# Kernel tuning notes

Measured on AMD Instinct MI355X. Metric: run time of the kernel, lower is better.

The kernel has to match this reference:

```python
import jax, jax.numpy as jnp
import numpy as np

B, M, N, L = 4096, 128, 96, 20


def setup_inputs() -> dict:
    key = jax.random.key(0)
    k1, k2, k3, k4 = jax.random.split(key, 4)
    x_ini = jax.random.normal(k1, (B, N, 1), jnp.float32)
    y = jax.random.normal(k2, (B, M, 1), jnp.float32)
    H = jax.random.normal(k3, (B, M, N), jnp.float32)
    xt = jax.random.normal(k4, (B, N, 1), jnp.float32)
    # learned parameters, initialized exactly as in the torch __init__
    grad_ss = jnp.full((L,), 0.001, jnp.float32)
    extra = []
    t = 1.0
    for _ in range(L):
        t1 = (1.0 + np.sqrt(1.0 + 4.0 * t * t)) / 2.0
        extra.append((t - 1.0) / t1)
        t = t1
    extra_ss = jnp.asarray(np.array(extra, dtype=np.float32))
    gamma1 = jnp.asarray(np.array([(5.0 - 0.1) / L * i + 0.1 for i in range(L)], dtype=np.float32))
    return {"x_ini": x_ini, "y": y, "H": H, "xt": xt,
            "grad_ss": grad_ss, "extra_ss": extra_ss, "gamma1": gamma1}


def reference(x_ini, y, H, xt, grad_ss, extra_ss, gamma1):
    central = jnp.array([-2.0, 0.0, 2.0], dtype=x_ini.dtype)  # 3-point codebook
    HTH = jnp.einsum('bmn,bmk->bnk', H, H)   # [B,N,N]
    HTy = jnp.einsum('bmn,bmk->bnk', H, y)   # [B,N,1]

    def step(carry, params):
        x, y_x = carry
        gs, es, gm = params
        grad_f = 2.0 * (jnp.matmul(HTH, y_x) - HTy)          # [B,N,1]
        x_buff = y_x - gs * grad_f                            # [B,N,1]
        # nearest-center lookup over the 3-entry codebook
        idx = jnp.argmin(jnp.abs(x_buff - central[None, None, :]), axis=2)  # [B,N]
        center = central[idx][..., None]                      # [B,N,1]
        ply = 2.0 * jax.nn.sigmoid(gm * (x_buff - center)) - 1.0
        y_x_new = ply + es * (ply - x)                        # FISTA momentum
        return (ply, y_x_new), None

    (x, _), _ = jax.lax.scan(step, (x_ini, x_ini), (grad_ss, extra_ss, gamma1))
    d = x - xt
    loss = jnp.sum(d * d).reshape(1, 1)  # sum_b (x-xt)^T (x-xt)
    return x, loss
```

## Files before the change

### kernel.cpp

```cpp
#include <hip/hip_runtime.h>

#define NB 4096
#define MM 128
#define NN 96
#define LL 20

typedef __attribute__((ext_vector_type(8))) short bf16x8;
typedef __attribute__((ext_vector_type(4))) float f32x4;
typedef __attribute__((ext_vector_type(4))) unsigned int u32x4;

#define UT_STRIDE 72

__device__ __forceinline__ unsigned short rne16(float f) {
    unsigned u = __float_as_uint(f);
    return (unsigned short)((u + 0x7fffu + ((u >> 16) & 1u)) >> 16);
}
__device__ __forceinline__ unsigned pack2(float a, float b) {
    return (unsigned)rne16(a) | ((unsigned)rne16(b) << 16);
}
__device__ __forceinline__ float bperm_f(int srcB, float v) {
    return __int_as_float(__builtin_amdgcn_ds_bpermute(srcB, __float_as_int(v)));
}

__global__ __launch_bounds__(64) __attribute__((amdgpu_waves_per_eu(2)))
void pg_kernel(const float* __restrict__ x_ini,
               const float* __restrict__ y,
               const float* __restrict__ H,
               const float* __restrict__ xt,
               const float* __restrict__ grad_ss,
               const float* __restrict__ extra_ss,
               const float* __restrict__ gamma1,
               float* __restrict__ out)
{
    __shared__ __align__(16) unsigned short Ut[112 * UT_STRIDE];
    __shared__ __align__(16) unsigned yxL[48];
    __shared__ float par[3][LL];

    const int b    = blockIdx.x;
    const int lane = threadIdx.x;
    const int m15  = lane & 15;
    const int g4   = lane >> 4;

    if (lane < LL) {
        par[0][lane] = grad_ss[lane];
        par[1][lane] = extra_ss[lane];
        par[2][lane] = gamma1[lane];
    }
    {
        unsigned* U32 = (unsigned*)Ut;
        #pragma unroll
        for (int i = 97 * (UT_STRIDE / 2) + lane; i < 112 * (UT_STRIDE / 2); i += 64)
            U32[i] = 0;
    }

    f32x4 acc[6][7];
    #pragma unroll
    for (int I = 0; I < 6; ++I)
        #pragma unroll
        for (int J = 0; J < 7; ++J)
            #pragma unroll
            for (int r = 0; r < 4; ++r) acc[I][J][r] = 0.f;

    const float* Hb = H + (size_t)b * (MM * NN);
    for (int kh = 0; kh < 2; ++kh) {
        if (kh) __syncthreads();
        const float* rsrc = Hb + (size_t)(kh * 64 + lane) * NN;
        #pragma unroll
        for (int ch = 0; ch < 4; ++ch) {
            float4 v[6];
            #pragma unroll
            for (int i = 0; i < 6; ++i) v[i] = *(const float4*)(rsrc + ch * 24 + 4 * i);
            #pragma unroll
            for (int i = 0; i < 6; ++i) {
                const int c = ch * 24 + 4 * i;
                Ut[(c + 0) * UT_STRIDE + lane] = rne16(v[i].x);
                Ut[(c + 1) * UT_STRIDE + lane] = rne16(v[i].y);
                Ut[(c + 2) * UT_STRIDE + lane] = rne16(v[i].z);
                Ut[(c + 3) * UT_STRIDE + lane] = rne16(v[i].w);
            }
        }
        Ut[96 * UT_STRIDE + lane] = rne16(y[(size_t)b * MM + kh * 64 + lane]);
        __syncthreads();

        #pragma unroll
        for (int s = 0; s < 2; ++s) {
            bf16x8 fr[7];
            #pragma unroll
            for (int T = 0; T < 7; ++T)
                fr[T] = *(const bf16x8*)&Ut[(T * 16 + m15) * UT_STRIDE + s * 32 + g4 * 8];
            #pragma unroll
            for (int I = 0; I < 6; ++I)
                #pragma unroll
                for (int J = 0; J < 7; ++J)
                    acc[I][J] = __builtin_amdgcn_mfma_f32_16x16x32_bf16(fr[I], fr[J], acc[I][J], 0, 0, 0);
        }
    }

    unsigned pk[6][6][2];
    #pragma unroll
    for (int I = 0; I < 6; ++I)
        #pragma unroll
        for (int J = 0; J < 6; ++J) {
            pk[I][J][0] = pack2(acc[I][J][0], acc[I][J][1]);
            pk[I][J][1] = pack2(acc[I][J][2], acc[I][J][3]);
        }
    const int srcL[2] = { (m15 + 16 * (2 * (g4 & 1) + 0)) << 2,
                          (m15 + 16 * (2 * (g4 & 1) + 1)) << 2 };
    const bool hiHalf = (g4 >> 1) != 0;
    bf16x8 afr[6][3];
    #pragma unroll
    for (int Ip = 0; Ip < 6; ++Ip)
        #pragma unroll
        for (int kk = 0; kk < 3; ++kk) {
            u32x4 w;
            #pragma unroll
            for (int p = 0; p < 4; ++p) {
                int va = __builtin_amdgcn_ds_bpermute(srcL[p >> 1], (int)pk[2 * kk][Ip][p & 1]);
                int vb = __builtin_amdgcn_ds_bpermute(srcL[p >> 1], (int)pk[2 * kk + 1][Ip][p & 1]);
                w[p] = (unsigned)(hiHalf ? vb : va);
            }
            afr[Ip][kk] = __builtin_bit_cast(bf16x8, w);
        }
    float hty4[4];
    {
        const int srcC = (16 * g4) << 2;
        #pragma unroll
        for (int r = 0; r < 4; ++r) {
            float v0 = bperm_f(srcC, acc[0][6][r]);
            float v1 = bperm_f(srcC, acc[1][6][r]);
            float v2 = bperm_f(srcC, acc[2][6][r]);
            float v3 = bperm_f(srcC, acc[3][6][r]);
            float v4 = bperm_f(srcC, acc[4][6][r]);
            float v5 = bperm_f(srcC, acc[5][6][r]);
            float s = v0;
            s = (m15 == 1) ? v1 : s;
            s = (m15 == 2) ? v2 : s;
            s = (m15 == 3) ? v3 : s;
            s = (m15 == 4) ? v4 : s;
            s = (m15 == 5) ? v5 : s;
            hty4[r] = s;
        }
    }

    const bool wr = (m15 < 6);
    const int  rb = m15 * 16 + g4 * 4;
    float yx4[4] = {0, 0, 0, 0}, xc4[4] = {0, 0, 0, 0};
    if (wr) {
        float4 xi = *(const float4*)(x_ini + (size_t)b * NN + rb);
        yx4[0] = xi.x; yx4[1] = xi.y; yx4[2] = xi.z; yx4[3] = xi.w;
        xc4[0] = xi.x; xc4[1] = xi.y; xc4[2] = xi.z; xc4[3] = xi.w;
        yxL[(rb >> 1) + 0] = pack2(yx4[0], yx4[1]);
        yxL[(rb >> 1) + 1] = pack2(yx4[2], yx4[3]);
    }
    __syncthreads();

    for (int t = 0; t < LL; ++t) {
        bf16x8 bf[3];
        #pragma unroll
        for (int kk = 0; kk < 3; ++kk)
            bf[kk] = *(const bf16x8*)&yxL[kk * 16 + g4 * 4];
        f32x4 aD[6];
        #pragma unroll
        for (int Ip = 0; Ip < 6; ++Ip)
            #pragma unroll
            for (int r = 0; r < 4; ++r) aD[Ip][r] = 0.f;
        #pragma unroll
        for (int kk = 0; kk < 3; ++kk)
            #pragma unroll
            for (int Ip = 0; Ip < 6; ++Ip)
                aD[Ip] = __builtin_amdgcn_mfma_f32_16x16x32_bf16(afr[Ip][kk], bf[kk], aD[Ip], 0, 0, 0);
        f32x4 am = aD[0];
        am = (m15 == 1) ? aD[1] : am;
        am = (m15 == 2) ? aD[2] : am;
        am = (m15 == 3) ? aD[3] : am;
        am = (m15 == 4) ? aD[4] : am;
        am = (m15 == 5) ? aD[5] : am;

        if (wr) {
            const float gs = par[0][t], es = par[1][t], gmv = par[2][t];
            #pragma unroll
            for (int r = 0; r < 4; ++r) {
                float xb  = fmaf(-2.0f * gs, am[r] - hty4[r], yx4[r]);
                float cen = 2.0f * fminf(fmaxf(rintf(xb * 0.5f), -1.0f), 1.0f);
                float z   = gmv * (xb - cen);
                float e   = __expf(-z);
                float ply = fmaf(2.0f, __builtin_amdgcn_rcpf(1.0f + e), -1.0f);
                float yxn = fmaf(es, ply - xc4[r], ply);
                xc4[r] = ply;
                yx4[r] = yxn;
            }
            if (t + 1 < LL) {
                yxL[(rb >> 1) + 0] = pack2(yx4[0], yx4[1]);
                yxL[(rb >> 1) + 1] = pack2(yx4[2], yx4[3]);
            }
        }
        __syncthreads();
    }

    float part = 0.f;
    if (wr) {
        float4 xo;
        xo.x = xc4[0]; xo.y = xc4[1]; xo.z = xc4[2]; xo.w = xc4[3];
        *(float4*)(out + (size_t)b * NN + rb) = xo;
        float4 xr = *(const float4*)(xt + (size_t)b * NN + rb);
        float d0 = xc4[0] - xr.x, d1 = xc4[1] - xr.y;
        float d2 = xc4[2] - xr.z, d3 = xc4[3] - xr.w;
        part = (d0 * d0 + d1 * d1) + (d2 * d2 + d3 * d3);
    }
    #pragma unroll
    for (int m = 1; m < 64; m <<= 1) part += __shfl_xor(part, m, 64);
    if (lane == 0) atomicAdd(out + (size_t)NB * NN, part);
}

extern "C" void kernel_launch(void* const* d_in, const int* in_sizes, int n_in,
                              void* d_out, int out_size, void* d_ws, size_t ws_size,
                              hipStream_t stream) {
    const float* x_ini    = (const float*)d_in[0];
    const float* y        = (const float*)d_in[1];
    const float* H        = (const float*)d_in[2];
    const float* xt       = (const float*)d_in[3];
    const float* grad_ss  = (const float*)d_in[4];
    const float* extra_ss = (const float*)d_in[5];
    const float* gamma1   = (const float*)d_in[6];
    float* out = (float*)d_out;

    hipMemsetAsync(out + (size_t)NB * NN, 0, sizeof(float), stream);
    pg_kernel<<<NB, 64, 0, stream>>>(x_ini, y, H, xt, grad_ss, extra_ss, gamma1, out);
}
```

Before: 96.23 us.

## Split per-batch Gram and iteration work across two waves per block

Each block now runs 128 threads (two waves). Each wave computes half of the HTH columns plus HTy through MFMA, then holds only its half of the matrix fragments for the 20 iterations. The y_x vector is double-buffered in shared memory so one barrier per iteration is enough across the waves. HTy now passes through shared memory instead of bpermute shuffles. This cuts per-wave MFMA and register load and should raise occupancy, at the cost of a cross-wave barrier in every iteration and duplicated A-fragment loads.

```diff
diff --git a/kernel.cpp b/kernel.cpp
--- a/kernel.cpp
+++ b/kernel.cpp
@@ -4,13 +4,12 @@
 #define MM 128
 #define NN 96
 #define LL 20
+#define UTS 72
 
 typedef __attribute__((ext_vector_type(8))) short bf16x8;
 typedef __attribute__((ext_vector_type(4))) float f32x4;
 typedef __attribute__((ext_vector_type(4))) unsigned int u32x4;
 
-#define UT_STRIDE 72
-
 __device__ __forceinline__ unsigned short rne16(float f) {
     unsigned u = __float_as_uint(f);
     return (unsigned short)((u + 0x7fffu + ((u >> 16) & 1u)) >> 16);
@@ -18,11 +17,8 @@
 __device__ __forceinline__ unsigned pack2(float a, float b) {
     return (unsigned)rne16(a) | ((unsigned)rne16(b) << 16);
 }
-__device__ __forceinline__ float bperm_f(int srcB, float v) {
-    return __int_as_float(__builtin_amdgcn_ds_bpermute(srcB, __float_as_int(v)));
-}
-
-__global__ __launch_bounds__(64) __attribute__((amdgpu_waves_per_eu(2)))
+
+__global__ __launch_bounds__(128) __attribute__((amdgpu_waves_per_eu(3)))
 void pg_kernel(const float* __restrict__ x_ini,
                const float* __restrict__ y,
                const float* __restrict__ H,
@@ -32,149 +28,150 @@
                const float* __restrict__ gamma1,
                float* __restrict__ out)
 {
-    __shared__ __align__(16) unsigned short Ut[112 * UT_STRIDE];
-    __shared__ __align__(16) unsigned yxL[48];
+    __shared__ __align__(16) unsigned short Ut[97 * UTS];
+    __shared__ __align__(16) unsigned yxD[2][48];
+    __shared__ __align__(16) float htyL[NN];
     __shared__ float par[3][LL];
 
     const int b    = blockIdx.x;
-    const int lane = threadIdx.x;
+    const int tid  = threadIdx.x;
+    const int lane = tid & 63;
+    const int wid  = tid >> 6;
     const int m15  = lane & 15;
     const int g4   = lane >> 4;
 
-    if (lane < LL) {
-        par[0][lane] = grad_ss[lane];
-        par[1][lane] = extra_ss[lane];
-        par[2][lane] = gamma1[lane];
-    }
-    {
-        unsigned* U32 = (unsigned*)Ut;
-        #pragma unroll
-        for (int i = 97 * (UT_STRIDE / 2) + lane; i < 112 * (UT_STRIDE / 2); i += 64)
-            U32[i] = 0;
-    }
-
-    f32x4 acc[6][7];
-    #pragma unroll
-    for (int I = 0; I < 6; ++I)
-        #pragma unroll
-        for (int J = 0; J < 7; ++J)
-            #pragma unroll
-            for (int r = 0; r < 4; ++r) acc[I][J][r] = 0.f;
-
-    const float* Hb = H + (size_t)b * (MM * NN);
+    if (tid < LL) {
+        par[0][tid] = grad_ss[tid];
+        par[1][tid] = extra_ss[tid];
+        par[2][tid] = gamma1[tid];
+    }
+
+    f32x4 acc[6][3];
+    f32x4 accY[6];
+    #pragma unroll
+    for (int kt = 0; kt < 6; ++kt) {
+        #pragma unroll
+        for (int jl = 0; jl < 3; ++jl)
+            #pragma unroll
+            for (int r = 0; r < 4; ++r) acc[kt][jl][r] = 0.f;
+        #pragma unroll
+        for (int r = 0; r < 4; ++r) accY[kt][r] = 0.f;
+    }
+
+    const float* Hb  = H + (size_t)b * (MM * NN);
+    const int    r64 = tid >> 1;
+    const int    qh  = tid & 1;
+
     for (int kh = 0; kh < 2; ++kh) {
         if (kh) __syncthreads();
-        const float* rsrc = Hb + (size_t)(kh * 64 + lane) * NN;
-        #pragma unroll
-        for (int ch = 0; ch < 4; ++ch) {
-            float4 v[6];
-            #pragma unroll
-            for (int i = 0; i < 6; ++i) v[i] = *(const float4*)(rsrc + ch * 24 + 4 * i);
-            #pragma unroll
-            for (int i = 0; i < 6; ++i) {
-                const int c = ch * 24 + 4 * i;
-                Ut[(c + 0) * UT_STRIDE + lane] = rne16(v[i].x);
-                Ut[(c + 1) * UT_STRIDE + lane] = rne16(v[i].y);
-                Ut[(c + 2) * UT_STRIDE + lane] = rne16(v[i].z);
-                Ut[(c + 3) * UT_STRIDE + lane] = rne16(v[i].w);
-            }
-        }
-        Ut[96 * UT_STRIDE + lane] = rne16(y[(size_t)b * MM + kh * 64 + lane]);
+        {
+            const float* src = Hb + (size_t)(kh * 64 + r64) * NN + qh * 48;
+            #pragma unroll
+            for (int c4 = 0; c4 < 3; ++c4) {
+                float4 v[4];
+                #pragma unroll
+                for (int i = 0; i < 4; ++i) v[i] = *(const float4*)(src + c4 * 16 + 4 * i);
+                #pragma unroll
+                for (int i = 0; i < 4; ++i) {
+                    const int c = qh * 48 + c4 * 16 + 4 * i;
+                    Ut[(c + 0) * UTS + r64] = rne16(v[i].x);
+                    Ut[(c + 1) * UTS + r64] = rne16(v[i].y);
+                    Ut[(c + 2) * UTS + r64] = rne16(v[i].z);
+                    Ut[(c + 3) * UTS + r64] = rne16(v[i].w);
+                }
+            }
+            if (tid < 64) Ut[96 * UTS + tid] = rne16(y[(size_t)b * MM + kh * 64 + tid]);
+        }
         __syncthreads();
 
         #pragma unroll
         for (int s = 0; s < 2; ++s) {
-            bf16x8 fr[7];
-            #pragma unroll
-            for (int T = 0; T < 7; ++T)
-                fr[T] = *(const bf16x8*)&Ut[(T * 16 + m15) * UT_STRIDE + s * 32 + g4 * 8];
-            #pragma unroll
-            for (int I = 0; I < 6; ++I)
+            const int ko = s * 32 + g4 * 8;
+            bf16x8 frB[3];
+            #pragma unroll
+            for (int jl = 0; jl < 3; ++jl)
+                frB[jl] = *(const bf16x8*)&Ut[((wid * 3 + jl) * 16 + m15) * UTS + ko];
+            bf16x8 frY = *(const bf16x8*)&Ut[96 * UTS + ko];
+            #pragma unroll
+            for (int kt = 0; kt < 6; ++kt) {
+                bf16x8 fa = *(const bf16x8*)&Ut[(kt * 16 + m15) * UTS + ko];
                 #pragma unroll
-                for (int J = 0; J < 7; ++J)
-                    acc[I][J] = __builtin_amdgcn_mfma_f32_16x16x32_bf16(fr[I], fr[J], acc[I][J], 0, 0, 0);
-        }
-    }
-
-    unsigned pk[6][6][2];
-    #pragma unroll
-    for (int I = 0; I < 6; ++I)
-        #pragma unroll
-        for (int J = 0; J < 6; ++J) {
-            pk[I][J][0] = pack2(acc[I][J][0], acc[I][J][1]);
-            pk[I][J][1] = pack2(acc[I][J][2], acc[I][J][3]);
+                for (int jl = 0; jl < 3; ++jl)
+                    acc[kt][jl] = __builtin_amdgcn_mfma_f32_16x16x32_bf16(fa, frB[jl], acc[kt][jl], 0, 0, 0);
+                accY[kt] = __builtin_amdgcn_mfma_f32_16x16x32_bf16(fa, frY, accY[kt], 0, 0, 0);
+            }
+        }
+    }
+
+    unsigned pk[6][3][2];
+    #pragma unroll
+    for (int kt = 0; kt < 6; ++kt)
+        #pragma unroll
+        for (int jl = 0; jl < 3; ++jl) {
+            pk[kt][jl][0] = pack2(acc[kt][jl][0], acc[kt][jl][1]);
+            pk[kt][jl][1] = pack2(acc[kt][jl][2], acc[kt][jl][3]);
         }
     const int srcL[2] = { (m15 + 16 * (2 * (g4 & 1) + 0)) << 2,
                           (m15 + 16 * (2 * (g4 & 1) + 1)) << 2 };
     const bool hiHalf = (g4 >> 1) != 0;
-    bf16x8 afr[6][3];
-    #pragma unroll
-    for (int Ip = 0; Ip < 6; ++Ip)
+    bf16x8 afr[3][3];
+    #pragma unroll
+    for (int jl = 0; jl < 3; ++jl)
         #pragma unroll
         for (int kk = 0; kk < 3; ++kk) {
             u32x4 w;
             #pragma unroll
             for (int p = 0; p < 4; ++p) {
-                int va = __builtin_amdgcn_ds_bpermute(srcL[p >> 1], (int)pk[2 * kk][Ip][p & 1]);
-                int vb = __builtin_amdgcn_ds_bpermute(srcL[p >> 1], (int)pk[2 * kk + 1][Ip][p & 1]);
+                int va = __builtin_amdgcn_ds_bpermute(srcL[p >> 1], (int)pk[2 * kk][jl][p & 1]);
+                int vb = __builtin_amdgcn_ds_bpermute(srcL[p >> 1], (int)pk[2 * kk + 1][jl][p & 1]);
                 w[p] = (unsigned)(hiHalf ? vb : va);
             }
-            afr[Ip][kk] = __builtin_bit_cast(bf16x8, w);
-        }
-    float hty4[4];
-    {
-        const int srcC = (16 * g4) << 2;
-        #pragma unroll
-        for (int r = 0; r < 4; ++r) {
-            float v0 = bperm_f(srcC, acc[0][6][r]);
-            float v1 = bperm_f(srcC, acc[1][6][r]);
-            float v2 = bperm_f(srcC, acc[2][6][r]);
-            float v3 = bperm_f(srcC, acc[3][6][r]);
-            float v4 = bperm_f(srcC, acc[4][6][r]);
-            float v5 = bperm_f(srcC, acc[5][6][r]);
-            float s = v0;
-            s = (m15 == 1) ? v1 : s;
-            s = (m15 == 2) ? v2 : s;
-            s = (m15 == 3) ? v3 : s;
-            s = (m15 == 4) ? v4 : s;
-            s = (m15 == 5) ? v5 : s;
-            hty4[r] = s;
-        }
-    }
-
-    const bool wr = (m15 < 6);
-    const int  rb = m15 * 16 + g4 * 4;
-    float yx4[4] = {0, 0, 0, 0}, xc4[4] = {0, 0, 0, 0};
+            afr[jl][kk] = __builtin_bit_cast(bf16x8, w);
+        }
+
+    if (wid == 0 && m15 == 0) {
+        #pragma unroll
+        for (int kt = 0; kt < 6; ++kt)
+            #pragma unroll
+            for (int r = 0; r < 4; ++r)
+                htyL[kt * 16 + g4 * 4 + r] = accY[kt][r];
+    }
+
+    const bool wr = (m15 < 3);
+    const int  rb = wid * 48 + m15 * 16 + g4 * 4;
+    float yx4[4] = {0, 0, 0, 0}, xc4[4] = {0, 0, 0, 0}, hty4[4] = {0, 0, 0, 0};
     if (wr) {
         float4 xi = *(const float4*)(x_ini + (size_t)b * NN + rb);
         yx4[0] = xi.x; yx4[1] = xi.y; yx4[2] = xi.z; yx4[3] = xi.w;
         xc4[0] = xi.x; xc4[1] = xi.y; xc4[2] = xi.z; xc4[3] = xi.w;
-        yxL[(rb >> 1) + 0] = pack2(yx4[0], yx4[1]);
-        yxL[(rb >> 1) + 1] = pack2(yx4[2], yx4[3]);
+        yxD[0][(rb >> 1) + 0] = pack2(yx4[0], yx4[1]);
+        yxD[0][(rb >> 1) + 1] = pack2(yx4[2], yx4[3]);
     }
     __syncthreads();
-
+    if (wr) {
+        float4 ht = *(const float4*)&htyL[rb];
+        hty4[0] = ht.x; hty4[1] = ht.y; hty4[2] = ht.z; hty4[3] = ht.w;
+    }
+
+    int cur = 0;
     for (int t = 0; t < LL; ++t) {
         bf16x8 bf[3];
         #pragma unroll
         for (int kk = 0; kk < 3; ++kk)
-            bf[kk] = *(const bf16x8*)&yxL[kk * 16 + g4 * 4];
-        f32x4 aD[6];
-        #pragma unroll
-        for (int Ip = 0; Ip < 6; ++Ip)
-            #pragma unroll
-            for (int r = 0; r < 4; ++r) aD[Ip][r] = 0.f;
+            bf[kk] = *(const bf16x8*)&yxD[cur][kk * 16 + g4 * 4];
+        f32x4 aD[3];
+        #pragma unroll
+        for (int jl = 0; jl < 3; ++jl)
+            #pragma unroll
+            for (int r = 0; r < 4; ++r) aD[jl][r] = 0.f;
         #pragma unroll
         for (int kk = 0; kk < 3; ++kk)
             #pragma unroll
-            for (int Ip = 0; Ip < 6; ++Ip)
-                aD[Ip] = __builtin_amdgcn_mfma_f32_16x16x32_bf16(afr[Ip][kk], bf[kk], aD[Ip], 0, 0, 0);
+            for (int jl = 0; jl < 3; ++jl)
+                aD[jl] = __builtin_amdgcn_mfma_f32_16x16x32_bf16(afr[jl][kk], bf[kk], aD[jl], 0, 0, 0);
         f32x4 am = aD[0];
         am = (m15 == 1) ? aD[1] : am;
         am = (m15 == 2) ? aD[2] : am;
-        am = (m15 == 3) ? aD[3] : am;
-        am = (m15 == 4) ? aD[4] : am;
-        am = (m15 == 5) ? aD[5] : am;
 
         if (wr) {
             const float gs = par[0][t], es = par[1][t], gmv = par[2][t];
@@ -190,11 +187,12 @@
                 yx4[r] = yxn;
             }
             if (t + 1 < LL) {
-                yxL[(rb >> 1) + 0] = pack2(yx4[0], yx4[1]);
-                yxL[(rb >> 1) + 1] = pack2(yx4[2], yx4[3]);
+                yxD[cur ^ 1][(rb >> 1) + 0] = pack2(yx4[0], yx4[1]);
+                yxD[cur ^ 1][(rb >> 1) + 1] = pack2(yx4[2], yx4[3]);
             }
         }
         __syncthreads();
+        cur ^= 1;
     }
 
     float part = 0.f;
@@ -225,5 +223,5 @@
     float* out = (float*)d_out;
 
     hipMemsetAsync(out + (size_t)NB * NN, 0, sizeof(float), stream);
-    pg_kernel<<<NB, 64, 0, stream>>>(x_ini, y, H, xt, grad_ss, extra_ss, gamma1, out);
-}
+    pg_kernel<<<NB, 128, 0, stream>>>(x_ini, y, H, xt, grad_ss, extra_ss, gamma1, out);
+}
```

New measurement: 158.2 us. +64.4%, slower.
